# Kernel optimization log

Hardware: AMD Instinct MI355X
Metric: run time of the kernel (lower is better)

## Reference

```python
import math
import jax, jax.numpy as jnp
import numpy as np

SIN_DIM = 8
HEADS = 4
HID = 64
EMBED = 6 + 1 + 3 * SIN_DIM + 5 + 2  # 38


def _sinusoidal(v):
    # v: [N] -> [N, SIN_DIM], interleaved sin/cos as in torch.stack(...).flatten(-2)
    div = jnp.exp(jnp.arange(0, SIN_DIM, 2, dtype=jnp.float32) * (-math.log(10000.0) / SIN_DIM))
    scaled = v[:, None] * div  # [N, SIN_DIM//2]
    return jnp.stack([jnp.sin(scaled), jnp.cos(scaled)], axis=-1).reshape(v.shape[0], SIN_DIM)


def _feature_embed(x):
    nt = jnp.clip(x[:, 0].astype(jnp.int32), 0, 5)
    role = jnp.clip(x[:, 5].astype(jnp.int32), 0, 4)
    return jnp.concatenate([
        jax.nn.one_hot(nt, 6, dtype=x.dtype),
        jnp.log1p(x[:, 1])[:, None],
        _sinusoidal(x[:, 2]),
        _sinusoidal(x[:, 3]),
        _sinusoidal(x[:, 4] * 100.0),
        jax.nn.one_hot(role, 5, dtype=x.dtype),
        x[:, 6:7],
        x[:, 7:8],
    ], axis=-1)  # [N, 38]


def _gat(x, adj, W, a_src, a_dst, concat):
    N = x.shape[0]
    h = (x @ W).reshape(N, HEADS, HID)                       # [N,H,D]
    src = jnp.einsum('nhd,hd->nh', h, a_src)                 # [N,H]
    dst = jnp.einsum('nhd,hd->nh', h, a_dst)                 # [N,H]
    e = src[:, None, :] + dst[None, :, :]                    # [N,N,H]
    e = jnp.where(e > 0, e, 0.2 * e)                         # leaky_relu(0.2)
    e = jnp.where(adj[:, :, None] > 0, e, -jnp.inf)
    a = jax.nn.softmax(e, axis=1)                            # softmax over neighbors j
    out = jnp.einsum('njh,nhd->nhd'.replace('nj', 'ij').replace('nhd,', 'jhd,').replace('->nhd', '->ihd'), a, h) if False else jnp.einsum('ijh,jhd->ihd', a, h)
    if concat:
        return out.reshape(N, HEADS * HID)
    return out.mean(axis=1)


def _layernorm(x, g, b, eps=1e-5):
    mu = x.mean(axis=-1, keepdims=True)
    var = ((x - mu) ** 2).mean(axis=-1, keepdims=True)
    return (x - mu) / jnp.sqrt(var + eps) * g + b


def setup_inputs() -> dict:
    key = jax.random.key(0)
    ks = jax.random.split(key, 16)
    N, C = 4096, 512
    # raw node features per FeatureEmbedding docstring
    nt = jax.random.randint(ks[0], (N,), 0, 6).astype(jnp.float32)
    arity = jax.random.randint(ks[1], (N,), 0, 5).astype(jnp.float32)
    arg_pos = jax.random.randint(ks[2], (N,), 0, 8).astype(jnp.float32)
    depth = jax.random.randint(ks[3], (N,), 0, 12).astype(jnp.float32)
    age = jax.random.uniform(ks[4], (N,))
    role = jax.random.randint(ks[5], (N,), 0, 5).astype(jnp.float32)
    pol = jax.random.bernoulli(ks[6], 0.5, (N,)).astype(jnp.float32)
    eq = jax.random.bernoulli(ks[7], 0.2, (N,)).astype(jnp.float32)
    node_features = jnp.stack([nt, arity, arg_pos, depth, age, role, pol, eq], axis=-1)
    adj = (jax.random.uniform(ks[8], (N, N)) < 0.01).astype(jnp.float32)
    adj = jnp.maximum(adj, jnp.eye(N, dtype=jnp.float32))  # self-loops
    pm = (jax.random.uniform(ks[9], (C, N)) < (8.0 / N)).astype(jnp.float32)
    pool_matrix = pm / jnp.clip(pm.sum(axis=1, keepdims=True), 1.0, None)
    def xavier(k, shape):
        fan = shape[0] + shape[-1]
        return jax.random.normal(k, shape, dtype=jnp.float32) * math.sqrt(2.0 / fan)
    return {
        'node_features': node_features, 'adj': adj, 'pool_matrix': pool_matrix,
        'W1': xavier(ks[10], (EMBED, HID * HEADS)),
        'a_src1': xavier(ks[11], (HEADS, HID)), 'a_dst1': xavier(ks[12], (HEADS, HID)),
        'g1': jnp.ones((HID * HEADS,), jnp.float32), 'b1': jnp.zeros((HID * HEADS,), jnp.float32),
        'W2': xavier(ks[13], (HID * HEADS, HID * HEADS)),
        'a_src2': xavier(ks[14], (HEADS, HID)), 'a_dst2': xavier(ks[15], (HEADS, HID)),
        'g2': jnp.ones((HID,), jnp.float32), 'b2': jnp.zeros((HID,), jnp.float32),
        'Ws': xavier(jax.random.fold_in(key, 100), (HID, HID)), 'bs': jnp.zeros((HID,), jnp.float32),
        'Wo': xavier(jax.random.fold_in(key, 101), (HID, 1)), 'bo': jnp.zeros((1,), jnp.float32),
    }


def reference(node_features, adj, pool_matrix, W1, a_src1, a_dst1, g1, b1,
              W2, a_src2, a_dst2, g2, b2, Ws, bs, Wo, bo):
    x = _feature_embed(node_features)                         # [N, 38]
    # layer 1: concat heads -> [N, 256]
    x = jax.nn.elu(_layernorm(_gat(x, adj, W1, a_src1, a_dst1, True), g1, b1))
    # layer 2: mean over heads -> [N, 64]  (dropout is eval-mode no-op)
    x = jax.nn.elu(_layernorm(_gat(x, adj, W2, a_src2, a_dst2, False), g2, b2))
    clause_emb = pool_matrix @ x                               # [C, 64]
    h = jax.nn.relu(clause_emb @ Ws + bs)                      # MLP scorer
    return (h @ Wo + bo)[:, 0]                                 # [C]
```

## Files before the change

### kernel.cpp

```cpp
#include <hip/hip_runtime.h>
#include <math.h>

#define N 4096
#define C 512
#define EMB 38
#define HEADS 4
#define HID 64
#define F1 256
#define MAXN 128
#define RPB 8

__device__ __forceinline__ float wr_sum(float v) {
#pragma unroll
    for (int o = 32; o > 0; o >>= 1) v += __shfl_xor(v, o);
    return v;
}
__device__ __forceinline__ float wr_max(float v) {
#pragma unroll
    for (int o = 32; o > 0; o >>= 1) v = fmaxf(v, __shfl_xor(v, o));
    return v;
}

__global__ __launch_bounds__(256) void k_gemm1(const float* __restrict__ nf, const float* __restrict__ W1,
                                               const float* __restrict__ asrc, const float* __restrict__ adst,
                                               float* __restrict__ h1, float* __restrict__ s1, float* __restrict__ d1) {
    int n0 = blockIdx.x * RPB, tid = threadIdx.x;
    __shared__ float fs[RPB][8];
    __shared__ float xs[RPB][40];
    if (tid < RPB * 8) fs[tid >> 3][tid & 7] = nf[(size_t)n0 * 8 + tid];
    if (tid < RPB * 2) xs[tid >> 1][38 + (tid & 1)] = 0.f;
    __syncthreads();
    {
        int r = tid & 7;
        int t = tid >> 3;
        const float* f = fs[r];
        for (int pass = 0; pass < 2; ++pass, t += 32) {
            if (t >= EMB) break;
            float val;
            if (t < 6) { int nt = min(max((int)f[0], 0), 5); val = (t == nt) ? 1.f : 0.f; }
            else if (t == 6) val = log1pf(f[1]);
            else if (t < 31) {
                int q = (t - 7) & 7, s = (t - 7) >> 3, m = q >> 1;
                float base = (s == 0) ? f[2] : (s == 1) ? f[3] : f[4] * 100.f;
                float div = expf((2.f * m) * (-logf(10000.f) / 8.f));
                float sc = base * div;
                val = (q & 1) ? cosf(sc) : sinf(sc);
            }
            else if (t < 36) { int role = min(max((int)f[5], 0), 4); val = (t - 31 == role) ? 1.f : 0.f; }
            else val = (t == 36) ? f[6] : f[7];
            xs[r][t] = val;
        }
    }
    __syncthreads();
    float acc[RPB];
#pragma unroll
    for (int r = 0; r < RPB; ++r) acc[r] = 0.f;
#pragma unroll
    for (int kk = 0; kk < 9; ++kk) {
        float w0 = W1[(4 * kk + 0) * F1 + tid];
        float w1 = W1[(4 * kk + 1) * F1 + tid];
        float w2 = W1[(4 * kk + 2) * F1 + tid];
        float w3 = W1[(4 * kk + 3) * F1 + tid];
#pragma unroll
        for (int r = 0; r < RPB; ++r) {
            float4 x = *(const float4*)&xs[r][4 * kk];
            acc[r] = fmaf(x.x, w0, fmaf(x.y, w1, fmaf(x.z, w2, fmaf(x.w, w3, acc[r]))));
        }
    }
#pragma unroll
    for (int k = 36; k < EMB; ++k) {
        float wvv = W1[k * F1 + tid];
#pragma unroll
        for (int r = 0; r < RPB; ++r) acc[r] = fmaf(xs[r][k], wvv, acc[r]);
    }
    int h = tid >> 6, lane = tid & 63;
    float av = asrc[tid], dv = adst[tid];
#pragma unroll
    for (int r = 0; r < RPB; ++r) {
        h1[(size_t)(n0 + r) * F1 + tid] = acc[r];
        float ss = wr_sum(acc[r] * av);
        float dd = wr_sum(acc[r] * dv);
        if (lane == 0) { s1[(n0 + r) * HEADS + h] = ss; d1[(n0 + r) * HEADS + h] = dd; }
    }
}

__global__ __launch_bounds__(256) void k_agg1(const float* __restrict__ adj, int* __restrict__ cnt,
                                              int* __restrict__ idx,
                                              const float* __restrict__ h1, const float* __restrict__ s1,
                                              const float* __restrict__ d1, const float* __restrict__ g,
                                              const float* __restrict__ b, float* __restrict__ xo) {
    int i = blockIdx.x, tid = threadIdx.x;
    int wv = tid >> 6, lane = tid & 63;
    __shared__ int nbrs[MAXN];
    __shared__ int wcnt[4];
    __shared__ float wts[HEADS][MAXN + 1];
    __shared__ float lsum[HEADS];
    __shared__ float sacc[4][F1];
    __shared__ float red[HEADS];

    const float* row = adj + (size_t)i * N;
    float v[16];
#pragma unroll
    for (int k = 0; k < 16; ++k) v[k] = row[wv * 1024 + k * 64 + lane];
    unsigned long long m[16];
    int tot = 0;
#pragma unroll
    for (int k = 0; k < 16; ++k) { m[k] = __ballot(v[k] > 0.f); tot += __popcll(m[k]); }
    if (lane == 0) wcnt[wv] = tot;
    __syncthreads();
    int base = 0;
#pragma unroll
    for (int w = 0; w < 4; ++w) if (w < wv) base += wcnt[w];
    int total = wcnt[0] + wcnt[1] + wcnt[2] + wcnt[3];
    int c = min(total, MAXN);
    unsigned long long below = (1ull << lane) - 1;
    int off = base;
#pragma unroll
    for (int k = 0; k < 16; ++k) {
        if (v[k] > 0.f) {
            int p = off + __popcll(m[k] & below);
            if (p < MAXN) {
                int col = wv * 1024 + k * 64 + lane;
                nbrs[p] = col;
                idx[i * MAXN + p] = col;
            }
        }
        off += __popcll(m[k]);
    }
    if (tid == 0) cnt[i] = c;
    __syncthreads();

    if (tid < c) {
        float4 dd = ((const float4*)d1)[nbrs[tid]];
        float4 ss = ((const float4*)s1)[i];
        float e0 = ss.x + dd.x, e1 = ss.y + dd.y, e2 = ss.z + dd.z, e3 = ss.w + dd.w;
        wts[0][tid] = e0 > 0.f ? e0 : 0.2f * e0;
        wts[1][tid] = e1 > 0.f ? e1 : 0.2f * e1;
        wts[2][tid] = e2 > 0.f ? e2 : 0.2f * e2;
        wts[3][tid] = e3 > 0.f ? e3 : 0.2f * e3;
    }
    __syncthreads();
    {
        float mm = -INFINITY;
        for (int jj = lane; jj < c; jj += 64) mm = fmaxf(mm, wts[wv][jj]);
        mm = wr_max(mm);
        float l = 0.f;
        for (int jj = lane; jj < c; jj += 64) { float t = expf(wts[wv][jj] - mm); wts[wv][jj] = t; l += t; }
        l = wr_sum(l);
        if (lane == 0) lsum[wv] = l;
    }
    __syncthreads();
    int hq = lane >> 4;
    const float4* hv = (const float4*)h1;
    float4 acc = {0.f, 0.f, 0.f, 0.f};
    int jj = wv;
    for (; jj + 12 < c; jj += 16) {
        int na = nbrs[jj], nb = nbrs[jj + 4], nc = nbrs[jj + 8], nd = nbrs[jj + 12];
        float wa = wts[hq][jj], wb = wts[hq][jj + 4], wc = wts[hq][jj + 8], wd = wts[hq][jj + 12];
        float4 va = hv[(size_t)na * 64 + lane];
        float4 vb = hv[(size_t)nb * 64 + lane];
        float4 vc = hv[(size_t)nc * 64 + lane];
        float4 vd = hv[(size_t)nd * 64 + lane];
        acc.x = fmaf(wa, va.x, acc.x); acc.y = fmaf(wa, va.y, acc.y);
        acc.z = fmaf(wa, va.z, acc.z); acc.w = fmaf(wa, va.w, acc.w);
        acc.x = fmaf(wb, vb.x, acc.x); acc.y = fmaf(wb, vb.y, acc.y);
        acc.z = fmaf(wb, vb.z, acc.z); acc.w = fmaf(wb, vb.w, acc.w);
        acc.x = fmaf(wc, vc.x, acc.x); acc.y = fmaf(wc, vc.y, acc.y);
        acc.z = fmaf(wc, vc.z, acc.z); acc.w = fmaf(wc, vc.w, acc.w);
        acc.x = fmaf(wd, vd.x, acc.x); acc.y = fmaf(wd, vd.y, acc.y);
        acc.z = fmaf(wd, vd.z, acc.z); acc.w = fmaf(wd, vd.w, acc.w);
    }
    for (; jj < c; jj += 4) {
        int na = nbrs[jj];
        float wa = wts[hq][jj];
        float4 va = hv[(size_t)na * 64 + lane];
        acc.x = fmaf(wa, va.x, acc.x); acc.y = fmaf(wa, va.y, acc.y);
        acc.z = fmaf(wa, va.z, acc.z); acc.w = fmaf(wa, va.w, acc.w);
    }
    ((float4*)&sacc[wv][0])[lane] = acc;
    __syncthreads();
    float totv = (sacc[0][tid] + sacc[1][tid] + sacc[2][tid] + sacc[3][tid]) / lsum[wv];
    float s = wr_sum(totv);
    if (lane == 0) red[wv] = s;
    __syncthreads();
    float mu = (red[0] + red[1] + red[2] + red[3]) * (1.f / F1);
    float dvv = totv - mu;
    float s2 = wr_sum(dvv * dvv);
    __syncthreads();
    if (lane == 0) red[wv] = s2;
    __syncthreads();
    float var = (red[0] + red[1] + red[2] + red[3]) * (1.f / F1);
    float y = dvv * rsqrtf(var + 1e-5f) * g[tid] + b[tid];
    xo[(size_t)i * F1 + tid] = y > 0.f ? y : expm1f(y);
}

__global__ __launch_bounds__(256) void k_gemm2(const float* __restrict__ x1, const float* __restrict__ W2,
                                               const float* __restrict__ asrc, const float* __restrict__ adst,
                                               float* __restrict__ h2, float* __restrict__ s2, float* __restrict__ d2) {
    int n0 = blockIdx.x * RPB, tid = threadIdx.x;
    __shared__ float4 xs4[RPB][F1 / 4];
    {
        int r = tid >> 5, kk = tid & 31;
        const float4* x1v = (const float4*)x1;
        xs4[r][kk]      = x1v[(size_t)(n0 + r) * 64 + kk];
        xs4[r][kk + 32] = x1v[(size_t)(n0 + r) * 64 + kk + 32];
    }
    __syncthreads();
    float acc[RPB];
#pragma unroll
    for (int r = 0; r < RPB; ++r) acc[r] = 0.f;
    for (int kk = 0; kk < F1 / 4; ++kk) {
        float w0 = W2[(4 * kk + 0) * F1 + tid];
        float w1 = W2[(4 * kk + 1) * F1 + tid];
        float w2 = W2[(4 * kk + 2) * F1 + tid];
        float w3 = W2[(4 * kk + 3) * F1 + tid];
#pragma unroll
        for (int r = 0; r < RPB; ++r) {
            float4 x = xs4[r][kk];
            acc[r] = fmaf(x.x, w0, fmaf(x.y, w1, fmaf(x.z, w2, fmaf(x.w, w3, acc[r]))));
        }
    }
    int h = tid >> 6, lane = tid & 63;
    float av = asrc[tid], dv = adst[tid];
#pragma unroll
    for (int r = 0; r < RPB; ++r) {
        h2[(size_t)(n0 + r) * F1 + tid] = acc[r];
        float ss = wr_sum(acc[r] * av);
        float dd = wr_sum(acc[r] * dv);
        if (lane == 0) { s2[(n0 + r) * HEADS + h] = ss; d2[(n0 + r) * HEADS + h] = dd; }
    }
}

__global__ __launch_bounds__(256) void k_agg2(const float* __restrict__ h2, const float* __restrict__ s2,
                                              const float* __restrict__ d2, const int* __restrict__ cnt,
                                              const int* __restrict__ idx, const float* __restrict__ g,
                                              const float* __restrict__ b, float* __restrict__ xo) {
    int i = blockIdx.x, tid = threadIdx.x;
    int wv = tid >> 6, lane = tid & 63;
    __shared__ int nbrs[MAXN];
    __shared__ float wts[HEADS][MAXN + 1];
    __shared__ float lsum[HEADS];
    __shared__ float sacc[4][F1];
    int c = cnt[i];
    if (tid < c) nbrs[tid] = idx[i * MAXN + tid];
    __syncthreads();
    if (tid < c) {
        float4 dd = ((const float4*)d2)[nbrs[tid]];
        float4 ss = ((const float4*)s2)[i];
        float e0 = ss.x + dd.x, e1 = ss.y + dd.y, e2 = ss.z + dd.z, e3 = ss.w + dd.w;
        wts[0][tid] = e0 > 0.f ? e0 : 0.2f * e0;
        wts[1][tid] = e1 > 0.f ? e1 : 0.2f * e1;
        wts[2][tid] = e2 > 0.f ? e2 : 0.2f * e2;
        wts[3][tid] = e3 > 0.f ? e3 : 0.2f * e3;
    }
    __syncthreads();
    {
        float m = -INFINITY;
        for (int jj = lane; jj < c; jj += 64) m = fmaxf(m, wts[wv][jj]);
        m = wr_max(m);
        float l = 0.f;
        for (int jj = lane; jj < c; jj += 64) { float t = expf(wts[wv][jj] - m); wts[wv][jj] = t; l += t; }
        l = wr_sum(l);
        if (lane == 0) lsum[wv] = l;
    }
    __syncthreads();
    int hq = lane >> 4;
    const float4* hvv = (const float4*)h2;
    float4 acc = {0.f, 0.f, 0.f, 0.f};
    int jj = wv;
    for (; jj + 12 < c; jj += 16) {
        int na = nbrs[jj], nb = nbrs[jj + 4], nc = nbrs[jj + 8], nd = nbrs[jj + 12];
        float wa = wts[hq][jj], wb = wts[hq][jj + 4], wc = wts[hq][jj + 8], wd = wts[hq][jj + 12];
        float4 va = hvv[(size_t)na * 64 + lane];
        float4 vb = hvv[(size_t)nb * 64 + lane];
        float4 vc = hvv[(size_t)nc * 64 + lane];
        float4 vd = hvv[(size_t)nd * 64 + lane];
        acc.x = fmaf(wa, va.x, acc.x); acc.y = fmaf(wa, va.y, acc.y);
        acc.z = fmaf(wa, va.z, acc.z); acc.w = fmaf(wa, va.w, acc.w);
        acc.x = fmaf(wb, vb.x, acc.x); acc.y = fmaf(wb, vb.y, acc.y);
        acc.z = fmaf(wb, vb.z, acc.z); acc.w = fmaf(wb, vb.w, acc.w);
        acc.x = fmaf(wc, vc.x, acc.x); acc.y = fmaf(wc, vc.y, acc.y);
        acc.z = fmaf(wc, vc.z, acc.z); acc.w = fmaf(wc, vc.w, acc.w);
        acc.x = fmaf(wd, vd.x, acc.x); acc.y = fmaf(wd, vd.y, acc.y);
        acc.z = fmaf(wd, vd.z, acc.z); acc.w = fmaf(wd, vd.w, acc.w);
    }
    for (; jj < c; jj += 4) {
        int na = nbrs[jj];
        float wa = wts[hq][jj];
        float4 va = hvv[(size_t)na * 64 + lane];
        acc.x = fmaf(wa, va.x, acc.x); acc.y = fmaf(wa, va.y, acc.y);
        acc.z = fmaf(wa, va.z, acc.z); acc.w = fmaf(wa, va.w, acc.w);
    }
    ((float4*)&sacc[wv][0])[lane] = acc;
    __syncthreads();
    if (wv == 0) {
        float t0 = 0.f, t1 = 0.f, t2 = 0.f, t3 = 0.f;
#pragma unroll
        for (int w = 0; w < 4; ++w) {
            t0 += sacc[w][lane];
            t1 += sacc[w][lane + 64];
            t2 += sacc[w][lane + 128];
            t3 += sacc[w][lane + 192];
        }
        float mv = (t0 / lsum[0] + t1 / lsum[1] + t2 / lsum[2] + t3 / lsum[3]) * 0.25f;
        float mu = wr_sum(mv) * (1.f / HID);
        float dvv = mv - mu;
        float var = wr_sum(dvv * dvv) * (1.f / HID);
        float y = dvv * rsqrtf(var + 1e-5f) * g[lane] + b[lane];
        xo[i * HID + lane] = y > 0.f ? y : expm1f(y);
    }
}

__global__ __launch_bounds__(256) void k_poolscore(const float* __restrict__ pm, const float* __restrict__ x2,
                                                   const float* __restrict__ Ws, const float* __restrict__ bs,
                                                   const float* __restrict__ Wo, const float* __restrict__ bo,
                                                   float* __restrict__ out) {
    int c = blockIdx.x, tid = threadIdx.x;
    int w = tid >> 6, lane = tid & 63;
    __shared__ float sacc[4][HID];
    __shared__ float ce_s[HID];
    float acc = 0.f;
    const float4* pmv = (const float4*)(pm + (size_t)c * N);
#pragma unroll
    for (int it = 0; it < 4; ++it) {
        int vi = w * 256 + it * 64 + lane;
        float4 p4 = pmv[vi];
        float pc[4] = {p4.x, p4.y, p4.z, p4.w};
#pragma unroll
        for (int comp = 0; comp < 4; ++comp) {
            unsigned long long msk = __ballot(pc[comp] != 0.f);
            while (msk) {
                int bpos = __ffsll(msk) - 1;
                msk &= msk - 1;
                float pj = __shfl(pc[comp], bpos);
                int j = (w * 256 + it * 64 + bpos) * 4 + comp;
                acc += pj * x2[(size_t)j * HID + lane];
            }
        }
    }
    sacc[w][lane] = acc;
    __syncthreads();
    if (w == 0) ce_s[lane] = sacc[0][lane] + sacc[1][lane] + sacc[2][lane] + sacc[3][lane];
    __syncthreads();
    if (w == 0) {
        float hd = bs[lane];
#pragma unroll 8
        for (int k = 0; k < HID; ++k) hd = fmaf(ce_s[k], Ws[k * HID + lane], hd);
        hd = fmaxf(hd, 0.f);
        float v = wr_sum(hd * Wo[lane]);
        if (lane == 0) out[c] = v + bo[0];
    }
}

extern "C" void kernel_launch(void* const* d_in, const int* in_sizes, int n_in,
                              void* d_out, int out_size, void* d_ws, size_t ws_size,
                              hipStream_t stream) {
    const float* nf  = (const float*)d_in[0];
    const float* adj = (const float*)d_in[1];
    const float* pm  = (const float*)d_in[2];
    const float* W1  = (const float*)d_in[3];
    const float* as1 = (const float*)d_in[4];
    const float* ad1 = (const float*)d_in[5];
    const float* g1  = (const float*)d_in[6];
    const float* b1  = (const float*)d_in[7];
    const float* W2  = (const float*)d_in[8];
    const float* as2 = (const float*)d_in[9];
    const float* ad2 = (const float*)d_in[10];
    const float* g2  = (const float*)d_in[11];
    const float* b2  = (const float*)d_in[12];
    const float* Ws  = (const float*)d_in[13];
    const float* bs  = (const float*)d_in[14];
    const float* Wo  = (const float*)d_in[15];
    const float* bo  = (const float*)d_in[16];
    float* out = (float*)d_out;

    float* p = (float*)d_ws;
    float* h1  = p; p += (size_t)N * F1;
    float* s1  = p; p += (size_t)N * HEADS;
    float* d1  = p; p += (size_t)N * HEADS;
    float* x1  = p; p += (size_t)N * F1;
    float* h2  = p; p += (size_t)N * F1;
    float* s2  = p; p += (size_t)N * HEADS;
    float* d2  = p; p += (size_t)N * HEADS;
    float* x2  = p; p += (size_t)N * HID;
    int* cnt = (int*)p;
    int* idx = cnt + N;

    k_gemm1<<<N / RPB, 256, 0, stream>>>(nf, W1, as1, ad1, h1, s1, d1);
    k_agg1<<<N, 256, 0, stream>>>(adj, cnt, idx, h1, s1, d1, g1, b1, x1);
    k_gemm2<<<N / RPB, 256, 0, stream>>>(x1, W2, as2, ad2, h2, s2, d2);
    k_agg2<<<N, 256, 0, stream>>>(h2, s2, d2, cnt, idx, g2, b2, x2);
    k_poolscore<<<C, 256, 0, stream>>>(pm, x2, Ws, bs, Wo, bo, out);
}
```

Baseline: 195.9 us.

## Fuse all stages into one persistent kernel with atomic grid barriers

Replaces the five separate kernel launches with a single persistent kernel of 512 blocks. Each block processes 8 rows per stage, and the stages are separated by atomic-counter grid barriers. The adjacency scan is also split out of the layer-1 aggregation into its own pre-barrier phase. The intent is to remove launch gaps and tail effects between the small stages. In exchange, the kernel relies on all 512 blocks being co-resident, since it uses a plain launch rather than a cooperative one. It also loses per-row parallelism: N=4096 rows are processed serially 8 per block, where before there was one block per row.

After: 451.2 us. 130% more time.

```diff
diff --git a/kernel.cpp b/kernel.cpp
--- a/kernel.cpp
+++ b/kernel.cpp
@@ -9,6 +9,7 @@
 #define F1 256
 #define MAXN 128
 #define RPB 8
+#define GRID 512
 
 __device__ __forceinline__ float wr_sum(float v) {
 #pragma unroll
@@ -21,334 +22,352 @@
     return v;
 }
 
-__global__ __launch_bounds__(256) void k_gemm1(const float* __restrict__ nf, const float* __restrict__ W1,
-                                               const float* __restrict__ asrc, const float* __restrict__ adst,
-                                               float* __restrict__ h1, float* __restrict__ s1, float* __restrict__ d1) {
-    int n0 = blockIdx.x * RPB, tid = threadIdx.x;
-    __shared__ float fs[RPB][8];
-    __shared__ float xs[RPB][40];
-    if (tid < RPB * 8) fs[tid >> 3][tid & 7] = nf[(size_t)n0 * 8 + tid];
-    if (tid < RPB * 2) xs[tid >> 1][38 + (tid & 1)] = 0.f;
+__device__ __forceinline__ void gbar(int* ctr) {
     __syncthreads();
+    if (threadIdx.x == 0) {
+        __hip_atomic_fetch_add(ctr, 1, __ATOMIC_RELEASE, __HIP_MEMORY_SCOPE_AGENT);
+        while (__hip_atomic_load(ctr, __ATOMIC_ACQUIRE, __HIP_MEMORY_SCOPE_AGENT) < GRID)
+            __builtin_amdgcn_s_sleep(2);
+    }
+    __syncthreads();
+}
+
+__global__ __launch_bounds__(64) void k_zero(int* __restrict__ ctr) {
+    if (threadIdx.x < 4) ctr[threadIdx.x] = 0;
+}
+
+struct SGemm1 { float fs[RPB][8]; float xs[RPB][40]; };
+struct SAgg   { int nbrs[MAXN]; float wts[HEADS][MAXN + 1]; float lsum[HEADS]; float sacc[4][F1]; float red[HEADS]; };
+struct SGemm2 { float4 xs4[RPB][F1 / 4]; };
+struct SPool  { float sacc[4][HID]; float ce_s[HID]; };
+struct SScan  { int wcnt[4]; };
+union SMem { SGemm1 g1; SAgg a; SGemm2 g2; SPool p; SScan sc; };
+
+__global__ __launch_bounds__(256, 2) void k_mega(
+    const float* __restrict__ nf, const float* __restrict__ adj, const float* __restrict__ pm,
+    const float* __restrict__ W1, const float* __restrict__ as1, const float* __restrict__ ad1,
+    const float* __restrict__ g1, const float* __restrict__ b1,
+    const float* __restrict__ W2, const float* __restrict__ as2, const float* __restrict__ ad2,
+    const float* __restrict__ g2, const float* __restrict__ b2,
+    const float* __restrict__ Ws, const float* __restrict__ bs,
+    const float* __restrict__ Wo, const float* __restrict__ bo,
+    float* __restrict__ h1, float* __restrict__ s1, float* __restrict__ d1, float* __restrict__ x1,
+    float* __restrict__ h2, float* __restrict__ s2, float* __restrict__ d2, float* __restrict__ x2,
+    int* __restrict__ cnt, int* __restrict__ idx, int* __restrict__ ctr, float* __restrict__ out)
+{
+    int bid = blockIdx.x, tid = threadIdx.x;
+    int wv = tid >> 6, lane = tid & 63;
+    __shared__ SMem sm;
+
     {
-        int r = tid & 7;
-        int t = tid >> 3;
-        const float* f = fs[r];
-        for (int pass = 0; pass < 2; ++pass, t += 32) {
-            if (t >= EMB) break;
-            float val;
-            if (t < 6) { int nt = min(max((int)f[0], 0), 5); val = (t == nt) ? 1.f : 0.f; }
-            else if (t == 6) val = log1pf(f[1]);
-            else if (t < 31) {
-                int q = (t - 7) & 7, s = (t - 7) >> 3, m = q >> 1;
-                float base = (s == 0) ? f[2] : (s == 1) ? f[3] : f[4] * 100.f;
-                float div = expf((2.f * m) * (-logf(10000.f) / 8.f));
-                float sc = base * div;
-                val = (q & 1) ? cosf(sc) : sinf(sc);
-            }
-            else if (t < 36) { int role = min(max((int)f[5], 0), 4); val = (t - 31 == role) ? 1.f : 0.f; }
-            else val = (t == 36) ? f[6] : f[7];
-            xs[r][t] = val;
-        }
-    }
-    __syncthreads();
-    float acc[RPB];
-#pragma unroll
-    for (int r = 0; r < RPB; ++r) acc[r] = 0.f;
-#pragma unroll
-    for (int kk = 0; kk < 9; ++kk) {
-        float w0 = W1[(4 * kk + 0) * F1 + tid];
-        float w1 = W1[(4 * kk + 1) * F1 + tid];
-        float w2 = W1[(4 * kk + 2) * F1 + tid];
-        float w3 = W1[(4 * kk + 3) * F1 + tid];
+        int n0 = bid * RPB;
+        if (tid < RPB * 8) sm.g1.fs[tid >> 3][tid & 7] = nf[(size_t)n0 * 8 + tid];
+        if (tid < RPB * 2) sm.g1.xs[tid >> 1][38 + (tid & 1)] = 0.f;
+        __syncthreads();
+        {
+            int r = tid & 7;
+            int t = tid >> 3;
+            const float* f = sm.g1.fs[r];
+            for (int pass = 0; pass < 2; ++pass, t += 32) {
+                if (t >= EMB) break;
+                float val;
+                if (t < 6) { int nt = min(max((int)f[0], 0), 5); val = (t == nt) ? 1.f : 0.f; }
+                else if (t == 6) val = log1pf(f[1]);
+                else if (t < 31) {
+                    int q = (t - 7) & 7, s = (t - 7) >> 3, m = q >> 1;
+                    float base = (s == 0) ? f[2] : (s == 1) ? f[3] : f[4] * 100.f;
+                    float div = expf((2.f * m) * (-logf(10000.f) / 8.f));
+                    float sc = base * div;
+                    val = (q & 1) ? cosf(sc) : sinf(sc);
+                }
+                else if (t < 36) { int role = min(max((int)f[5], 0), 4); val = (t - 31 == role) ? 1.f : 0.f; }
+                else val = (t == 36) ? f[6] : f[7];
+                sm.g1.xs[r][t] = val;
+            }
+        }
+        __syncthreads();
+        float acc[RPB];
+#pragma unroll
+        for (int r = 0; r < RPB; ++r) acc[r] = 0.f;
+#pragma unroll
+        for (int kk = 0; kk < 9; ++kk) {
+            float w0 = W1[(4 * kk + 0) * F1 + tid];
+            float w1 = W1[(4 * kk + 1) * F1 + tid];
+            float w2 = W1[(4 * kk + 2) * F1 + tid];
+            float w3 = W1[(4 * kk + 3) * F1 + tid];
+#pragma unroll
+            for (int r = 0; r < RPB; ++r) {
+                float4 x = *(const float4*)&sm.g1.xs[r][4 * kk];
+                acc[r] = fmaf(x.x, w0, fmaf(x.y, w1, fmaf(x.z, w2, fmaf(x.w, w3, acc[r]))));
+            }
+        }
+#pragma unroll
+        for (int k = 36; k < EMB; ++k) {
+            float wvv = W1[k * F1 + tid];
+#pragma unroll
+            for (int r = 0; r < RPB; ++r) acc[r] = fmaf(sm.g1.xs[r][k], wvv, acc[r]);
+        }
+        int h = tid >> 6;
+        float av = as1[tid], dv = ad1[tid];
 #pragma unroll
         for (int r = 0; r < RPB; ++r) {
-            float4 x = *(const float4*)&xs[r][4 * kk];
-            acc[r] = fmaf(x.x, w0, fmaf(x.y, w1, fmaf(x.z, w2, fmaf(x.w, w3, acc[r]))));
-        }
-    }
-#pragma unroll
-    for (int k = 36; k < EMB; ++k) {
-        float wvv = W1[k * F1 + tid];
-#pragma unroll
-        for (int r = 0; r < RPB; ++r) acc[r] = fmaf(xs[r][k], wvv, acc[r]);
-    }
-    int h = tid >> 6, lane = tid & 63;
-    float av = asrc[tid], dv = adst[tid];
-#pragma unroll
-    for (int r = 0; r < RPB; ++r) {
-        h1[(size_t)(n0 + r) * F1 + tid] = acc[r];
-        float ss = wr_sum(acc[r] * av);
-        float dd = wr_sum(acc[r] * dv);
-        if (lane == 0) { s1[(n0 + r) * HEADS + h] = ss; d1[(n0 + r) * HEADS + h] = dd; }
-    }
-}
-
-__global__ __launch_bounds__(256) void k_agg1(const float* __restrict__ adj, int* __restrict__ cnt,
-                                              int* __restrict__ idx,
-                                              const float* __restrict__ h1, const float* __restrict__ s1,
-                                              const float* __restrict__ d1, const float* __restrict__ g,
-                                              const float* __restrict__ b, float* __restrict__ xo) {
-    int i = blockIdx.x, tid = threadIdx.x;
-    int wv = tid >> 6, lane = tid & 63;
-    __shared__ int nbrs[MAXN];
-    __shared__ int wcnt[4];
-    __shared__ float wts[HEADS][MAXN + 1];
-    __shared__ float lsum[HEADS];
-    __shared__ float sacc[4][F1];
-    __shared__ float red[HEADS];
-
-    const float* row = adj + (size_t)i * N;
-    float v[16];
-#pragma unroll
-    for (int k = 0; k < 16; ++k) v[k] = row[wv * 1024 + k * 64 + lane];
-    unsigned long long m[16];
-    int tot = 0;
-#pragma unroll
-    for (int k = 0; k < 16; ++k) { m[k] = __ballot(v[k] > 0.f); tot += __popcll(m[k]); }
-    if (lane == 0) wcnt[wv] = tot;
-    __syncthreads();
-    int base = 0;
-#pragma unroll
-    for (int w = 0; w < 4; ++w) if (w < wv) base += wcnt[w];
-    int total = wcnt[0] + wcnt[1] + wcnt[2] + wcnt[3];
-    int c = min(total, MAXN);
-    unsigned long long below = (1ull << lane) - 1;
-    int off = base;
-#pragma unroll
-    for (int k = 0; k < 16; ++k) {
-        if (v[k] > 0.f) {
-            int p = off + __popcll(m[k] & below);
-            if (p < MAXN) {
-                int col = wv * 1024 + k * 64 + lane;
-                nbrs[p] = col;
-                idx[i * MAXN + p] = col;
-            }
-        }
-        off += __popcll(m[k]);
-    }
-    if (tid == 0) cnt[i] = c;
-    __syncthreads();
-
-    if (tid < c) {
-        float4 dd = ((const float4*)d1)[nbrs[tid]];
-        float4 ss = ((const float4*)s1)[i];
-        float e0 = ss.x + dd.x, e1 = ss.y + dd.y, e2 = ss.z + dd.z, e3 = ss.w + dd.w;
-        wts[0][tid] = e0 > 0.f ? e0 : 0.2f * e0;
-        wts[1][tid] = e1 > 0.f ? e1 : 0.2f * e1;
-        wts[2][tid] = e2 > 0.f ? e2 : 0.2f * e2;
-        wts[3][tid] = e3 > 0.f ? e3 : 0.2f * e3;
-    }
-    __syncthreads();
+            h1[(size_t)(n0 + r) * F1 + tid] = acc[r];
+            float ss = wr_sum(acc[r] * av);
+            float dd = wr_sum(acc[r] * dv);
+            if (lane == 0) { s1[(n0 + r) * HEADS + h] = ss; d1[(n0 + r) * HEADS + h] = dd; }
+        }
+        __syncthreads();
+    }
+
     {
-        float mm = -INFINITY;
-        for (int jj = lane; jj < c; jj += 64) mm = fmaxf(mm, wts[wv][jj]);
-        mm = wr_max(mm);
-        float l = 0.f;
-        for (int jj = lane; jj < c; jj += 64) { float t = expf(wts[wv][jj] - mm); wts[wv][jj] = t; l += t; }
-        l = wr_sum(l);
-        if (lane == 0) lsum[wv] = l;
-    }
-    __syncthreads();
-    int hq = lane >> 4;
-    const float4* hv = (const float4*)h1;
-    float4 acc = {0.f, 0.f, 0.f, 0.f};
-    int jj = wv;
-    for (; jj + 12 < c; jj += 16) {
-        int na = nbrs[jj], nb = nbrs[jj + 4], nc = nbrs[jj + 8], nd = nbrs[jj + 12];
-        float wa = wts[hq][jj], wb = wts[hq][jj + 4], wc = wts[hq][jj + 8], wd = wts[hq][jj + 12];
-        float4 va = hv[(size_t)na * 64 + lane];
-        float4 vb = hv[(size_t)nb * 64 + lane];
-        float4 vc = hv[(size_t)nc * 64 + lane];
-        float4 vd = hv[(size_t)nd * 64 + lane];
-        acc.x = fmaf(wa, va.x, acc.x); acc.y = fmaf(wa, va.y, acc.y);
-        acc.z = fmaf(wa, va.z, acc.z); acc.w = fmaf(wa, va.w, acc.w);
-        acc.x = fmaf(wb, vb.x, acc.x); acc.y = fmaf(wb, vb.y, acc.y);
-        acc.z = fmaf(wb, vb.z, acc.z); acc.w = fmaf(wb, vb.w, acc.w);
-        acc.x = fmaf(wc, vc.x, acc.x); acc.y = fmaf(wc, vc.y, acc.y);
-        acc.z = fmaf(wc, vc.z, acc.z); acc.w = fmaf(wc, vc.w, acc.w);
-        acc.x = fmaf(wd, vd.x, acc.x); acc.y = fmaf(wd, vd.y, acc.y);
-        acc.z = fmaf(wd, vd.z, acc.z); acc.w = fmaf(wd, vd.w, acc.w);
-    }
-    for (; jj < c; jj += 4) {
-        int na = nbrs[jj];
-        float wa = wts[hq][jj];
-        float4 va = hv[(size_t)na * 64 + lane];
-        acc.x = fmaf(wa, va.x, acc.x); acc.y = fmaf(wa, va.y, acc.y);
-        acc.z = fmaf(wa, va.z, acc.z); acc.w = fmaf(wa, va.w, acc.w);
-    }
-    ((float4*)&sacc[wv][0])[lane] = acc;
-    __syncthreads();
-    float totv = (sacc[0][tid] + sacc[1][tid] + sacc[2][tid] + sacc[3][tid]) / lsum[wv];
-    float s = wr_sum(totv);
-    if (lane == 0) red[wv] = s;
-    __syncthreads();
-    float mu = (red[0] + red[1] + red[2] + red[3]) * (1.f / F1);
-    float dvv = totv - mu;
-    float s2 = wr_sum(dvv * dvv);
-    __syncthreads();
-    if (lane == 0) red[wv] = s2;
-    __syncthreads();
-    float var = (red[0] + red[1] + red[2] + red[3]) * (1.f / F1);
-    float y = dvv * rsqrtf(var + 1e-5f) * g[tid] + b[tid];
-    xo[(size_t)i * F1 + tid] = y > 0.f ? y : expm1f(y);
-}
-
-__global__ __launch_bounds__(256) void k_gemm2(const float* __restrict__ x1, const float* __restrict__ W2,
-                                               const float* __restrict__ asrc, const float* __restrict__ adst,
-                                               float* __restrict__ h2, float* __restrict__ s2, float* __restrict__ d2) {
-    int n0 = blockIdx.x * RPB, tid = threadIdx.x;
-    __shared__ float4 xs4[RPB][F1 / 4];
+        int row0 = bid * 8;
+        for (int r = 0; r < 8; ++r) {
+            int i = row0 + r;
+            const float* row = adj + (size_t)i * N;
+            float v[16];
+#pragma unroll
+            for (int k = 0; k < 16; ++k) v[k] = row[wv * 1024 + k * 64 + lane];
+            unsigned long long m[16];
+            int tot = 0;
+#pragma unroll
+            for (int k = 0; k < 16; ++k) { m[k] = __ballot(v[k] > 0.f); tot += __popcll(m[k]); }
+            if (lane == 0) sm.sc.wcnt[wv] = tot;
+            __syncthreads();
+            int base = 0;
+#pragma unroll
+            for (int w = 0; w < 4; ++w) if (w < wv) base += sm.sc.wcnt[w];
+            int total = sm.sc.wcnt[0] + sm.sc.wcnt[1] + sm.sc.wcnt[2] + sm.sc.wcnt[3];
+            unsigned long long below = (1ull << lane) - 1;
+            int off = base;
+#pragma unroll
+            for (int k = 0; k < 16; ++k) {
+                if (v[k] > 0.f) {
+                    int p = off + __popcll(m[k] & below);
+                    if (p < MAXN) idx[i * MAXN + p] = wv * 1024 + k * 64 + lane;
+                }
+                off += __popcll(m[k]);
+            }
+            if (tid == 0) cnt[i] = min(total, MAXN);
+            __syncthreads();
+        }
+    }
+    gbar(&ctr[0]);
+
+    for (int r = 0; r < 8; ++r) {
+        int i = bid * 8 + r;
+        int c = cnt[i];
+        if (tid < c) sm.a.nbrs[tid] = idx[i * MAXN + tid];
+        __syncthreads();
+        if (tid < c) {
+            float4 dd = ((const float4*)d1)[sm.a.nbrs[tid]];
+            float4 ss = ((const float4*)s1)[i];
+            float e0 = ss.x + dd.x, e1 = ss.y + dd.y, e2 = ss.z + dd.z, e3 = ss.w + dd.w;
+            sm.a.wts[0][tid] = e0 > 0.f ? e0 : 0.2f * e0;
+            sm.a.wts[1][tid] = e1 > 0.f ? e1 : 0.2f * e1;
+            sm.a.wts[2][tid] = e2 > 0.f ? e2 : 0.2f * e2;
+            sm.a.wts[3][tid] = e3 > 0.f ? e3 : 0.2f * e3;
+        }
+        __syncthreads();
+        {
+            float mm = -INFINITY;
+            for (int jj = lane; jj < c; jj += 64) mm = fmaxf(mm, sm.a.wts[wv][jj]);
+            mm = wr_max(mm);
+            float l = 0.f;
+            for (int jj = lane; jj < c; jj += 64) { float t = expf(sm.a.wts[wv][jj] - mm); sm.a.wts[wv][jj] = t; l += t; }
+            l = wr_sum(l);
+            if (lane == 0) sm.a.lsum[wv] = l;
+        }
+        __syncthreads();
+        int hq = lane >> 4;
+        const float4* hv = (const float4*)h1;
+        float4 acc = {0.f, 0.f, 0.f, 0.f};
+        int jj = wv;
+        for (; jj + 12 < c; jj += 16) {
+            int na = sm.a.nbrs[jj], nb = sm.a.nbrs[jj + 4], nc = sm.a.nbrs[jj + 8], nd = sm.a.nbrs[jj + 12];
+            float wa = sm.a.wts[hq][jj], wb = sm.a.wts[hq][jj + 4], wc = sm.a.wts[hq][jj + 8], wd = sm.a.wts[hq][jj + 12];
+            float4 va = hv[(size_t)na * 64 + lane];
+            float4 vb = hv[(size_t)nb * 64 + lane];
+            float4 vc = hv[(size_t)nc * 64 + lane];
+            float4 vd = hv[(size_t)nd * 64 + lane];
+            acc.x = fmaf(wa, va.x, acc.x); acc.y = fmaf(wa, va.y, acc.y);
+            acc.z = fmaf(wa, va.z, acc.z); acc.w = fmaf(wa, va.w, acc.w);
+            acc.x = fmaf(wb, vb.x, acc.x); acc.y = fmaf(wb, vb.y, acc.y);
+            acc.z = fmaf(wb, vb.z, acc.z); acc.w = fmaf(wb, vb.w, acc.w);
+            acc.x = fmaf(wc, vc.x, acc.x); acc.y = fmaf(wc, vc.y, acc.y);
+            acc.z = fmaf(wc, vc.z, acc.z); acc.w = fmaf(wc, vc.w, acc.w);
+            acc.x = fmaf(wd, vd.x, acc.x); acc.y = fmaf(wd, vd.y, acc.y);
+            acc.z = fmaf(wd, vd.z, acc.z); acc.w = fmaf(wd, vd.w, acc.w);
+        }
+        for (; jj < c; jj += 4) {
+            int na = sm.a.nbrs[jj];
+            float wa = sm.a.wts[hq][jj];
+            float4 va = hv[(size_t)na * 64 + lane];
+            acc.x = fmaf(wa, va.x, acc.x); acc.y = fmaf(wa, va.y, acc.y);
+            acc.z = fmaf(wa, va.z, acc.z); acc.w = fmaf(wa, va.w, acc.w);
+        }
+        ((float4*)&sm.a.sacc[wv][0])[lane] = acc;
+        __syncthreads();
+        float totv = (sm.a.sacc[0][tid] + sm.a.sacc[1][tid] + sm.a.sacc[2][tid] + sm.a.sacc[3][tid]) / sm.a.lsum[wv];
+        float s = wr_sum(totv);
+        if (lane == 0) sm.a.red[wv] = s;
+        __syncthreads();
+        float mu = (sm.a.red[0] + sm.a.red[1] + sm.a.red[2] + sm.a.red[3]) * (1.f / F1);
+        float dvv = totv - mu;
+        float s2v = wr_sum(dvv * dvv);
+        __syncthreads();
+        if (lane == 0) sm.a.red[wv] = s2v;
+        __syncthreads();
+        float var = (sm.a.red[0] + sm.a.red[1] + sm.a.red[2] + sm.a.red[3]) * (1.f / F1);
+        float y = dvv * rsqrtf(var + 1e-5f) * g1[tid] + b1[tid];
+        x1[(size_t)i * F1 + tid] = y > 0.f ? y : expm1f(y);
+        __syncthreads();
+    }
+    gbar(&ctr[1]);
+
     {
-        int r = tid >> 5, kk = tid & 31;
-        const float4* x1v = (const float4*)x1;
-        xs4[r][kk]      = x1v[(size_t)(n0 + r) * 64 + kk];
-        xs4[r][kk + 32] = x1v[(size_t)(n0 + r) * 64 + kk + 32];
-    }
-    __syncthreads();
-    float acc[RPB];
-#pragma unroll
-    for (int r = 0; r < RPB; ++r) acc[r] = 0.f;
-    for (int kk = 0; kk < F1 / 4; ++kk) {
-        float w0 = W2[(4 * kk + 0) * F1 + tid];
-        float w1 = W2[(4 * kk + 1) * F1 + tid];
-        float w2 = W2[(4 * kk + 2) * F1 + tid];
-        float w3 = W2[(4 * kk + 3) * F1 + tid];
+        int n0 = bid * RPB;
+        {
+            int r = tid >> 5, kk = tid & 31;
+            const float4* x1v = (const float4*)x1;
+            sm.g2.xs4[r][kk]      = x1v[(size_t)(n0 + r) * 64 + kk];
+            sm.g2.xs4[r][kk + 32] = x1v[(size_t)(n0 + r) * 64 + kk + 32];
+        }
+        __syncthreads();
+        float acc[RPB];
+#pragma unroll
+        for (int r = 0; r < RPB; ++r) acc[r] = 0.f;
+        for (int kk = 0; kk < F1 / 4; ++kk) {
+            float w0 = W2[(4 * kk + 0) * F1 + tid];
+            float w1 = W2[(4 * kk + 1) * F1 + tid];
+            float w2 = W2[(4 * kk + 2) * F1 + tid];
+            float w3 = W2[(4 * kk + 3) * F1 + tid];
+#pragma unroll
+            for (int r = 0; r < RPB; ++r) {
+                float4 x = sm.g2.xs4[r][kk];
+                acc[r] = fmaf(x.x, w0, fmaf(x.y, w1, fmaf(x.z, w2, fmaf(x.w, w3, acc[r]))));
+            }
+        }
+        int h = tid >> 6;
+        float av = as2[tid], dv = ad2[tid];
 #pragma unroll
         for (int r = 0; r < RPB; ++r) {
-            float4 x = xs4[r][kk];
-            acc[r] = fmaf(x.x, w0, fmaf(x.y, w1, fmaf(x.z, w2, fmaf(x.w, w3, acc[r]))));
-        }
-    }
-    int h = tid >> 6, lane = tid & 63;
-    float av = asrc[tid], dv = adst[tid];
-#pragma unroll
-    for (int r = 0; r < RPB; ++r) {
-        h2[(size_t)(n0 + r) * F1 + tid] = acc[r];
-        float ss = wr_sum(acc[r] * av);
-        float dd = wr_sum(acc[r] * dv);
-        if (lane == 0) { s2[(n0 + r) * HEADS + h] = ss; d2[(n0 + r) * HEADS + h] = dd; }
-    }
-}
-
-__global__ __launch_bounds__(256) void k_agg2(const float* __restrict__ h2, const float* __restrict__ s2,
-                                              const float* __restrict__ d2, const int* __restrict__ cnt,
-                                              const int* __restrict__ idx, const float* __restrict__ g,
-                                              const float* __restrict__ b, float* __restrict__ xo) {
-    int i = blockIdx.x, tid = threadIdx.x;
-    int wv = tid >> 6, lane = tid & 63;
-    __shared__ int nbrs[MAXN];
-    __shared__ float wts[HEADS][MAXN + 1];
-    __shared__ float lsum[HEADS];
-    __shared__ float sacc[4][F1];
-    int c = cnt[i];
-    if (tid < c) nbrs[tid] = idx[i * MAXN + tid];
-    __syncthreads();
-    if (tid < c) {
-        float4 dd = ((const float4*)d2)[nbrs[tid]];
-        float4 ss = ((const float4*)s2)[i];
-        float e0 = ss.x + dd.x, e1 = ss.y + dd.y, e2 = ss.z + dd.z, e3 = ss.w + dd.w;
-        wts[0][tid] = e0 > 0.f ? e0 : 0.2f * e0;
-        wts[1][tid] = e1 > 0.f ? e1 : 0.2f * e1;
-        wts[2][tid] = e2 > 0.f ? e2 : 0.2f * e2;
-        wts[3][tid] = e3 > 0.f ? e3 : 0.2f * e3;
-    }
-    __syncthreads();
+            h2[(size_t)(n0 + r) * F1 + tid] = acc[r];
+            float ss = wr_sum(acc[r] * av);
+            float dd = wr_sum(acc[r] * dv);
+            if (lane == 0) { s2[(n0 + r) * HEADS + h] = ss; d2[(n0 + r) * HEADS + h] = dd; }
+        }
+        __syncthreads();
+    }
+    gbar(&ctr[2]);
+
+    for (int r = 0; r < 8; ++r) {
+        int i = bid * 8 + r;
+        int c = cnt[i];
+        if (tid < c) sm.a.nbrs[tid] = idx[i * MAXN + tid];
+        __syncthreads();
+        if (tid < c) {
+            float4 dd = ((const float4*)d2)[sm.a.nbrs[tid]];
+            float4 ss = ((const float4*)s2)[i];
+            float e0 = ss.x + dd.x, e1 = ss.y + dd.y, e2 = ss.z + dd.z, e3 = ss.w + dd.w;
+            sm.a.wts[0][tid] = e0 > 0.f ? e0 : 0.2f * e0;
+            sm.a.wts[1][tid] = e1 > 0.f ? e1 : 0.2f * e1;
+            sm.a.wts[2][tid] = e2 > 0.f ? e2 : 0.2f * e2;
+            sm.a.wts[3][tid] = e3 > 0.f ? e3 : 0.2f * e3;
+        }
+        __syncthreads();
+        {
+            float mm = -INFINITY;
+            for (int jj = lane; jj < c; jj += 64) mm = fmaxf(mm, sm.a.wts[wv][jj]);
+            mm = wr_max(mm);
+            float l = 0.f;
+            for (int jj = lane; jj < c; jj += 64) { float t = expf(sm.a.wts[wv][jj] - mm); sm.a.wts[wv][jj] = t; l += t; }
+            l = wr_sum(l);
+            if (lane == 0) sm.a.lsum[wv] = l;
+        }
+        __syncthreads();
+        int hq = lane >> 4;
+        const float4* hvv = (const float4*)h2;
+        float4 acc = {0.f, 0.f, 0.f, 0.f};
+        int jj = wv;
+        for (; jj + 12 < c; jj += 16) {
+            int na = sm.a.nbrs[jj], nb = sm.a.nbrs[jj + 4], nc = sm.a.nbrs[jj + 8], nd = sm.a.nbrs[jj + 12];
+            float wa = sm.a.wts[hq][jj], wb = sm.a.wts[hq][jj + 4], wc = sm.a.wts[hq][jj + 8], wd = sm.a.wts[hq][jj + 12];
+            float4 va = hvv[(size_t)na * 64 + lane];
+            float4 vb = hvv[(size_t)nb * 64 + lane];
+            float4 vc = hvv[(size_t)nc * 64 + lane];
+            float4 vd = hvv[(size_t)nd * 64 + lane];
+            acc.x = fmaf(wa, va.x, acc.x); acc.y = fmaf(wa, va.y, acc.y);
+            acc.z = fmaf(wa, va.z, acc.z); acc.w = fmaf(wa, va.w, acc.w);
+            acc.x = fmaf(wb, vb.x, acc.x); acc.y = fmaf(wb, vb.y, acc.y);
+            acc.z = fmaf(wb, vb.z, acc.z); acc.w = fmaf(wb, vb.w, acc.w);
+            acc.x = fmaf(wc, vc.x, acc.x); acc.y = fmaf(wc, vc.y, acc.y);
+            acc.z = fmaf(wc, vc.z, acc.z); acc.w = fmaf(wc, vc.w, acc.w);
+            acc.x = fmaf(wd, vd.x, acc.x); acc.y = fmaf(wd, vd.y, acc.y);
+            acc.z = fmaf(wd, vd.z, acc.z); acc.w = fmaf(wd, vd.w, acc.w);
+        }
+        for (; jj < c; jj += 4) {
+            int na = sm.a.nbrs[jj];
+            float wa = sm.a.wts[hq][jj];
+            float4 va = hvv[(size_t)na * 64 + lane];
+            acc.x = fmaf(wa, va.x, acc.x); acc.y = fmaf(wa, va.y, acc.y);
+            acc.z = fmaf(wa, va.z, acc.z); acc.w = fmaf(wa, va.w, acc.w);
+        }
+        ((float4*)&sm.a.sacc[wv][0])[lane] = acc;
+        __syncthreads();
+        if (wv == 0) {
+            float t0 = 0.f, t1 = 0.f, t2 = 0.f, t3 = 0.f;
+#pragma unroll
+            for (int w = 0; w < 4; ++w) {
+                t0 += sm.a.sacc[w][lane];
+                t1 += sm.a.sacc[w][lane + 64];
+                t2 += sm.a.sacc[w][lane + 128];
+                t3 += sm.a.sacc[w][lane + 192];
+            }
+            float mv = (t0 / sm.a.lsum[0] + t1 / sm.a.lsum[1] + t2 / sm.a.lsum[2] + t3 / sm.a.lsum[3]) * 0.25f;
+            float mu = wr_sum(mv) * (1.f / HID);
+            float dvv = mv - mu;
+            float var = wr_sum(dvv * dvv) * (1.f / HID);
+            float y = dvv * rsqrtf(var + 1e-5f) * g2[lane] + b2[lane];
+            x2[i * HID + lane] = y > 0.f ? y : expm1f(y);
+        }
+        __syncthreads();
+    }
+    gbar(&ctr[3]);
+
     {
-        float m = -INFINITY;
-        for (int jj = lane; jj < c; jj += 64) m = fmaxf(m, wts[wv][jj]);
-        m = wr_max(m);
-        float l = 0.f;
-        for (int jj = lane; jj < c; jj += 64) { float t = expf(wts[wv][jj] - m); wts[wv][jj] = t; l += t; }
-        l = wr_sum(l);
-        if (lane == 0) lsum[wv] = l;
-    }
-    __syncthreads();
-    int hq = lane >> 4;
-    const float4* hvv = (const float4*)h2;
-    float4 acc = {0.f, 0.f, 0.f, 0.f};
-    int jj = wv;
-    for (; jj + 12 < c; jj += 16) {
-        int na = nbrs[jj], nb = nbrs[jj + 4], nc = nbrs[jj + 8], nd = nbrs[jj + 12];
-        float wa = wts[hq][jj], wb = wts[hq][jj + 4], wc = wts[hq][jj + 8], wd = wts[hq][jj + 12];
-        float4 va = hvv[(size_t)na * 64 + lane];
-        float4 vb = hvv[(size_t)nb * 64 + lane];
-        float4 vc = hvv[(size_t)nc * 64 + lane];
-        float4 vd = hvv[(size_t)nd * 64 + lane];
-        acc.x = fmaf(wa, va.x, acc.x); acc.y = fmaf(wa, va.y, acc.y);
-        acc.z = fmaf(wa, va.z, acc.z); acc.w = fmaf(wa, va.w, acc.w);
-        acc.x = fmaf(wb, vb.x, acc.x); acc.y = fmaf(wb, vb.y, acc.y);
-        acc.z = fmaf(wb, vb.z, acc.z); acc.w = fmaf(wb, vb.w, acc.w);
-        acc.x = fmaf(wc, vc.x, acc.x); acc.y = fmaf(wc, vc.y, acc.y);
-        acc.z = fmaf(wc, vc.z, acc.z); acc.w = fmaf(wc, vc.w, acc.w);
-        acc.x = fmaf(wd, vd.x, acc.x); acc.y = fmaf(wd, vd.y, acc.y);
-        acc.z = fmaf(wd, vd.z, acc.z); acc.w = fmaf(wd, vd.w, acc.w);
-    }
-    for (; jj < c; jj += 4) {
-        int na = nbrs[jj];
-        float wa = wts[hq][jj];
-        float4 va = hvv[(size_t)na * 64 + lane];
-        acc.x = fmaf(wa, va.x, acc.x); acc.y = fmaf(wa, va.y, acc.y);
-        acc.z = fmaf(wa, va.z, acc.z); acc.w = fmaf(wa, va.w, acc.w);
-    }
-    ((float4*)&sacc[wv][0])[lane] = acc;
-    __syncthreads();
-    if (wv == 0) {
-        float t0 = 0.f, t1 = 0.f, t2 = 0.f, t3 = 0.f;
-#pragma unroll
-        for (int w = 0; w < 4; ++w) {
-            t0 += sacc[w][lane];
-            t1 += sacc[w][lane + 64];
-            t2 += sacc[w][lane + 128];
-            t3 += sacc[w][lane + 192];
-        }
-        float mv = (t0 / lsum[0] + t1 / lsum[1] + t2 / lsum[2] + t3 / lsum[3]) * 0.25f;
-        float mu = wr_sum(mv) * (1.f / HID);
-        float dvv = mv - mu;
-        float var = wr_sum(dvv * dvv) * (1.f / HID);
-        float y = dvv * rsqrtf(var + 1e-5f) * g[lane] + b[lane];
-        xo[i * HID + lane] = y > 0.f ? y : expm1f(y);
-    }
-}
-
-__global__ __launch_bounds__(256) void k_poolscore(const float* __restrict__ pm, const float* __restrict__ x2,
-                                                   const float* __restrict__ Ws, const float* __restrict__ bs,
-                                                   const float* __restrict__ Wo, const float* __restrict__ bo,
-                                                   float* __restrict__ out) {
-    int c = blockIdx.x, tid = threadIdx.x;
-    int w = tid >> 6, lane = tid & 63;
-    __shared__ float sacc[4][HID];
-    __shared__ float ce_s[HID];
-    float acc = 0.f;
-    const float4* pmv = (const float4*)(pm + (size_t)c * N);
-#pragma unroll
-    for (int it = 0; it < 4; ++it) {
-        int vi = w * 256 + it * 64 + lane;
-        float4 p4 = pmv[vi];
-        float pc[4] = {p4.x, p4.y, p4.z, p4.w};
-#pragma unroll
-        for (int comp = 0; comp < 4; ++comp) {
-            unsigned long long msk = __ballot(pc[comp] != 0.f);
-            while (msk) {
-                int bpos = __ffsll(msk) - 1;
-                msk &= msk - 1;
-                float pj = __shfl(pc[comp], bpos);
-                int j = (w * 256 + it * 64 + bpos) * 4 + comp;
-                acc += pj * x2[(size_t)j * HID + lane];
-            }
-        }
-    }
-    sacc[w][lane] = acc;
-    __syncthreads();
-    if (w == 0) ce_s[lane] = sacc[0][lane] + sacc[1][lane] + sacc[2][lane] + sacc[3][lane];
-    __syncthreads();
-    if (w == 0) {
-        float hd = bs[lane];
+        int cc = bid;
+        int w = wv;
+        float acc = 0.f;
+        const float4* pmv = (const float4*)(pm + (size_t)cc * N);
+#pragma unroll
+        for (int it = 0; it < 4; ++it) {
+            int vi = w * 256 + it * 64 + lane;
+            float4 p4 = pmv[vi];
+            float pc[4] = {p4.x, p4.y, p4.z, p4.w};
+#pragma unroll
+            for (int comp = 0; comp < 4; ++comp) {
+                unsigned long long msk = __ballot(pc[comp] != 0.f);
+                while (msk) {
+                    int bpos = __ffsll(msk) - 1;
+                    msk &= msk - 1;
+                    float pj = __shfl(pc[comp], bpos);
+                    int j = (w * 256 + it * 64 + bpos) * 4 + comp;
+                    acc += pj * x2[(size_t)j * HID + lane];
+                }
+            }
+        }
+        sm.p.sacc[w][lane] = acc;
+        __syncthreads();
+        if (w == 0) sm.p.ce_s[lane] = sm.p.sacc[0][lane] + sm.p.sacc[1][lane] + sm.p.sacc[2][lane] + sm.p.sacc[3][lane];
+        __syncthreads();
+        if (w == 0) {
+            float hd = bs[lane];
 #pragma unroll 8
-        for (int k = 0; k < HID; ++k) hd = fmaf(ce_s[k], Ws[k * HID + lane], hd);
-        hd = fmaxf(hd, 0.f);
-        float v = wr_sum(hd * Wo[lane]);
-        if (lane == 0) out[c] = v + bo[0];
+            for (int k = 0; k < HID; ++k) hd = fmaf(sm.p.ce_s[k], Ws[k * HID + lane], hd);
+            hd = fmaxf(hd, 0.f);
+            float v = wr_sum(hd * Wo[lane]);
+            if (lane == 0) out[cc] = v + bo[0];
+        }
     }
 }
 
@@ -385,10 +404,18 @@
     float* x2  = p; p += (size_t)N * HID;
     int* cnt = (int*)p;
     int* idx = cnt + N;
-
-    k_gemm1<<<N / RPB, 256, 0, stream>>>(nf, W1, as1, ad1, h1, s1, d1);
-    k_agg1<<<N, 256, 0, stream>>>(adj, cnt, idx, h1, s1, d1, g1, b1, x1);
-    k_gemm2<<<N / RPB, 256, 0, stream>>>(x1, W2, as2, ad2, h2, s2, d2);
-    k_agg2<<<N, 256, 0, stream>>>(h2, s2, d2, cnt, idx, g2, b2, x2);
-    k_poolscore<<<C, 256, 0, stream>>>(pm, x2, Ws, bs, Wo, bo, out);
-}
+    int* ctr = idx + (size_t)N * MAXN;
+
+    k_zero<<<1, 64, 0, stream>>>(ctr);
+
+    void* kargs[] = {
+        (void*)&nf, (void*)&adj, (void*)&pm,
+        (void*)&W1, (void*)&as1, (void*)&ad1, (void*)&g1, (void*)&b1,
+        (void*)&W2, (void*)&as2, (void*)&ad2, (void*)&g2, (void*)&b2,
+        (void*)&Ws, (void*)&bs, (void*)&Wo, (void*)&bo,
+        (void*)&h1, (void*)&s1, (void*)&d1, (void*)&x1,
+        (void*)&h2, (void*)&s2, (void*)&d2, (void*)&x2,
+        (void*)&cnt, (void*)&idx, (void*)&ctr, (void*)&out
+    };
+    hipLaunchKernel((const void*)k_mega, dim3(GRID), dim3(256), kargs, 0, stream);
+}
```
